# Kernel tuning notes

Hardware: AMD Instinct MI355X
Metric: run time of the kernel (lower is better)

The kernel has to match this reference:

```python
import jax, jax.numpy as jnp
import numpy as np

B, L, V, H = 2, 2048, 1024, 16
HD = V // H  # head size 64
EPS = 1e-3   # keras LayerNormalization default


def setup_inputs() -> dict:
    key = jax.random.key(0)
    ks = jax.random.split(key, 10)
    scale = 1.0 / np.sqrt(V)
    return {
        "query": jax.random.normal(ks[0], (B, L, V), jnp.float32),
        "key_t": jax.random.normal(ks[1], (B, L, V), jnp.float32),
        "value": jax.random.normal(ks[2], (B, L, V), jnp.float32),
        "Wq": jax.random.normal(ks[3], (H, V, HD), jnp.float32) * scale,
        "Wk": jax.random.normal(ks[4], (H, V, HD), jnp.float32) * scale,
        "Wv": jax.random.normal(ks[5], (H, V, HD), jnp.float32) * scale,
        "gamma": jnp.ones((V,), jnp.float32),
        "beta": jnp.zeros((V,), jnp.float32),
        "query_mask": jax.random.randint(ks[6], (B, L), 0, 2, jnp.int32),
        "value_mask": jax.random.randint(ks[7], (B, L), 0, 2, jnp.int32),
    }


def reference(query, key_t, value, Wq, Wk, Wv, gamma, beta, query_mask, value_mask):
    qm = query_mask.astype(jnp.float32)  # (B,L)
    vm = value_mask.astype(jnp.float32)  # (B,L)

    # per-head no-bias Dense projections, batched over heads
    Q = jnp.einsum('blv,hvd->bhld', query, Wq)
    K = jnp.einsum('blv,hvd->bhld', key_t, Wk)
    Vh = jnp.einsum('blv,hvd->bhld', value, Wv)

    scores = jnp.einsum('bhld,bhmd->bhlm', Q, K) / jnp.sqrt(jnp.float32(HD))
    attn = jax.nn.softmax(scores, axis=-1)

    # post-softmax multiplicative masking (faithful to original)
    tri = jnp.tril(jnp.ones((L, L), jnp.float32))  # (L,L) causal
    attn = attn * tri[None, None, :, :]
    attn = attn * qm[:, None, :, None] * vm[:, None, None, :]

    heads = jnp.einsum('bhlm,bhmd->bhld', attn, Vh)
    x = heads.transpose(0, 2, 1, 3).reshape(B, L, V)  # concat heads

    # dropout is identity at inference
    y = x + query
    mu = jnp.mean(y, axis=-1, keepdims=True)
    var = jnp.mean((y - mu) ** 2, axis=-1, keepdims=True)
    return gamma * (y - mu) * jax.lax.rsqrt(var + EPS) + beta
```

## Files before the change

### kernel.cpp

```cpp
#include <hip/hip_runtime.h>
#include <math.h>

constexpr int NB = 2;
constexpr int SL = 2048;
constexpr int NV = 1024;
constexpr int NH = 16;
constexpr int DH = 64;
constexpr float LN_EPS = 1e-3f;

typedef __bf16 bf16_t;
typedef __bf16 v8bf __attribute__((ext_vector_type(8)));
typedef float  v4f  __attribute__((ext_vector_type(4)));

__device__ __forceinline__ v8bf cvt8(float4 a, float4 b) {
  v8bf v;
  v[0] = (bf16_t)a.x; v[1] = (bf16_t)a.y; v[2] = (bf16_t)a.z; v[3] = (bf16_t)a.w;
  v[4] = (bf16_t)b.x; v[5] = (bf16_t)b.y; v[6] = (bf16_t)b.z; v[7] = (bf16_t)b.w;
  return v;
}
__device__ __forceinline__ unsigned pack_bf16(float a, float b) {
  unsigned short ua = __builtin_bit_cast(unsigned short, (bf16_t)a);
  unsigned short ub = __builtin_bit_cast(unsigned short, (bf16_t)b);
  return (unsigned)ua | ((unsigned)ub << 16);
}
__device__ __forceinline__ void async_cp16(const void* g, void* l) {
  __builtin_amdgcn_global_load_lds(
      (const __attribute__((address_space(1))) unsigned int*)g,
      (__attribute__((address_space(3))) unsigned int*)l, 16, 0, 0);
}

__global__ __launch_bounds__(256)
void wcvt(const float* __restrict__ Wq, const float* __restrict__ Wk,
          const float* __restrict__ Wv, bf16_t* __restrict__ Wt) {
  __shared__ float ls[64][65];
  const int z = blockIdx.z;
  const float* W = z == 0 ? Wq : (z == 1 ? Wk : Wv);
  const float sc = z == 0 ? 0.125f * 1.44269504f : 1.0f;
  const int h = blockIdx.y, v0 = blockIdx.x * 64;
  const int t = threadIdx.x;
  const int rr = t >> 4, c4 = t & 15;
  const float* src = W + ((size_t)h * NV + v0) * DH;
#pragma unroll
  for (int it = 0; it < 4; ++it) {
    float4 f = *(const float4*)(src + (size_t)(rr + it * 16) * DH + c4 * 4);
    ls[rr + it * 16][c4 * 4 + 0] = f.x;
    ls[rr + it * 16][c4 * 4 + 1] = f.y;
    ls[rr + it * 16][c4 * 4 + 2] = f.z;
    ls[rr + it * 16][c4 * 4 + 3] = f.w;
  }
  __syncthreads();
  const int dd = t >> 2, vq = t & 3;
  bf16_t tmp[16];
#pragma unroll
  for (int i = 0; i < 16; ++i) tmp[i] = (bf16_t)(ls[vq * 16 + i][dd] * sc);
  bf16_t* dst = Wt + ((size_t)z * NV + h * 64 + dd) * NV + v0 + vq * 16;
  *(v8bf*)dst = *(v8bf*)&tmp[0];
  *(v8bf*)(dst + 8) = *(v8bf*)&tmp[8];
}

__global__ __launch_bounds__(256, 3)
void proj_mfma(const float* __restrict__ A0, const float* __restrict__ A1,
               const float* __restrict__ A2, const bf16_t* __restrict__ Wtb,
               const int* __restrict__ vmask,
               bf16_t* __restrict__ O0, bf16_t* __restrict__ O1,
               bf16_t* __restrict__ O2) {
  __shared__ __align__(16) float  Asb[2][128 * 32];
  __shared__ __align__(16) bf16_t Wsb[2][128 * 32];

  const int z = blockIdx.z;
  const float*  A   = z == 0 ? A0 : (z == 1 ? A1 : A2);
  bf16_t*       out = z == 0 ? O0 : (z == 1 ? O1 : O2);
  const bf16_t* W   = Wtb + (size_t)z * NV * NV;

  const int t = threadIdx.x, w = t >> 6, lane = t & 63;
  const int g = lane >> 4, lx = lane & 15;
  const int m0 = blockIdx.x * 128, n0 = blockIdx.y * 128;
  const int rbase = (w >> 1) * 64, cbase = (w & 1) * 64;

  {
    const int ph = blockIdx.x % 3;
    if (ph == 1)      __builtin_amdgcn_s_sleep(26);
    else if (ph == 2) __builtin_amdgcn_s_sleep(52);
  }
  const int kph = blockIdx.x & 31;

  auto stageA = [&](int k0, int buf) {
#pragma unroll
    for (int s = 0; s < 4; ++s) {
      const int r = w * 32 + s * 8 + (lane >> 3);
      const int c = (lane & 7) ^ (r & 7);
      async_cp16(A + (size_t)(m0 + r) * NV + k0 + c * 4,
                 (char*)Asb[buf] + (w * 32 + s * 8) * 128);
    }
  };
  auto stageW = [&](int k0, int buf) {
#pragma unroll
    for (int s = 0; s < 2; ++s) {
      const int r = w * 32 + s * 16 + (lane >> 2);
      const int c = (lane & 3) ^ (r & 3);
      async_cp16(W + (size_t)(n0 + r) * NV + k0 + c * 8,
                 (char*)Wsb[buf] + (w * 32 + s * 16) * 64);
    }
  };
  auto kof = [&](int it) { return ((it + kph) & 31) * 32; };

  v4f acc[4][4] = {};
  stageA(kof(0), 0);
  stageW(kof(0), 0);

  for (int it = 0; it < 32; ++it) {
    const int buf = it & 1;
    __syncthreads();
    if (it < 31) { stageA(kof(it + 1), buf ^ 1); stageW(kof(it + 1), buf ^ 1); }
    v8bf af[4], wf[4];
#pragma unroll
    for (int rt = 0; rt < 4; ++rt) {
      const int row = rbase + rt * 16 + lx;
      const int sw = row & 7;
      float4 f0 = *(const float4*)((const char*)Asb[buf] + row * 128 + (((2 * g)     ^ sw) * 16));
      float4 f1 = *(const float4*)((const char*)Asb[buf] + row * 128 + (((2 * g + 1) ^ sw) * 16));
      af[rt] = cvt8(f0, f1);
    }
#pragma unroll
    for (int ct = 0; ct < 4; ++ct) {
      const int row = cbase + ct * 16 + lx;
      wf[ct] = *(const v8bf*)((const char*)Wsb[buf] + row * 64 +
                              ((g ^ (row & 3)) * 16));
    }
#pragma unroll
    for (int rt = 0; rt < 4; ++rt)
#pragma unroll
      for (int ct = 0; ct < 4; ++ct)
        acc[rt][ct] = __builtin_amdgcn_mfma_f32_16x16x32_bf16(
            af[rt], wf[ct], acc[rt][ct], 0, 0, 0);
  }

  if (z < 2) {
#pragma unroll
    for (int rt = 0; rt < 4; ++rt) {
#pragma unroll
      for (int reg = 0; reg < 4; ++reg) {
        const int row = m0 + rbase + rt * 16 + g * 4 + reg;
        const int b = row >> 11, l = row & (SL - 1);
#pragma unroll
        for (int ct = 0; ct < 4; ++ct) {
          const int n = n0 + cbase + ct * 16 + lx;
          const int h = n >> 6, d = n & 63;
          out[((size_t)(b * NH + h) * SL + l) * DH + d] = (bf16_t)acc[rt][ct][reg];
        }
      }
    }
  } else {
#pragma unroll
    for (int rt = 0; rt < 4; ++rt) {
      const int row = m0 + rbase + rt * 16 + g * 4;
      const int b = row >> 11, l = row & (SL - 1);
      float vm0 = (float)vmask[b * SL + l + 0];
      float vm1 = (float)vmask[b * SL + l + 1];
      float vm2 = (float)vmask[b * SL + l + 2];
      float vm3 = (float)vmask[b * SL + l + 3];
#pragma unroll
      for (int ct = 0; ct < 4; ++ct) {
        const int n = n0 + cbase + ct * 16 + lx;
        const int h = n >> 6, d = n & 63;
        uint2 u = {pack_bf16(acc[rt][ct][0] * vm0, acc[rt][ct][1] * vm1),
                   pack_bf16(acc[rt][ct][2] * vm2, acc[rt][ct][3] * vm3)};
        *(uint2*)&out[((size_t)(b * NH + h) * DH + d) * SL + l] = u;
      }
    }
  }
}

__global__ __launch_bounds__(256, 3)
void attn_mfma(const bf16_t* __restrict__ Qg, const bf16_t* __restrict__ Kg,
               const bf16_t* __restrict__ Vtg_all, const int* __restrict__ qmask,
               float* __restrict__ Xout) {
  __shared__ __align__(16) bf16_t kbuf[2][64 * 64];
  __shared__ __align__(16) bf16_t vbuf[2][64 * 64];
  __shared__ __align__(16) bf16_t Ps[4][32][72];

  const int id = blockIdx.x;
  const int bh = (id & 7) | ((id >> 7) << 3);
  const int qb = 15 - ((id >> 3) & 15);
  const int t = threadIdx.x, w = t >> 6, lane = t & 63;
  const int g = lane >> 4, lx = lane & 15;
  const int b = bh >> 4, h = bh & 15;
  const int l0 = qb * 128;
  const int lastAct = 2 * qb + 1;

  if ((id >> 3) & 1) __builtin_amdgcn_s_sleep(32);

  const bf16_t* Kb  = Kg + (size_t)bh * SL * DH;
  const bf16_t* Vtg = Vtg_all + (size_t)bh * DH * SL;

  v8bf qf[2][2];
#pragma unroll
  for (int qt = 0; qt < 2; ++qt)
#pragma unroll
    for (int ks = 0; ks < 2; ++ks)
      qf[qt][ks] = *(const v8bf*)&Qg[((size_t)bh * SL + l0 + w * 32 + qt * 16 + lx) * DH +
                                     ks * 32 + g * 8];

  v4f O[2][4] = {};
  float suml[2] = {0.f, 0.f};

  const int sr_off = lane >> 3, sc_l = lane & 7;
  auto stageK = [&](int mb, int buf) {
#pragma unroll
    for (int s = 0; s < 2; ++s) {
      const int r = w * 16 + s * 8 + sr_off;
      const int c = sc_l ^ (r & 7);
      async_cp16(Kb + (size_t)(mb + r) * DH + c * 8,
                 (char*)kbuf[buf] + (w * 16 + s * 8) * 128);
    }
  };
  auto stageV = [&](int mb, int buf) {
#pragma unroll
    for (int s = 0; s < 2; ++s) {
      const int r = w * 16 + s * 8 + sr_off;
      const int c = sc_l ^ (r & 7);
      async_cp16(Vtg + (size_t)r * SL + mb + c * 8,
                 (char*)vbuf[buf] + (w * 16 + s * 8) * 128);
    }
  };

  stageK(0, 0);
  stageV(0, 0);

  for (int mt = 0; mt <= lastAct; ++mt) {
    const int pb = mt & 1;
    __syncthreads();
    if (mt < SL / 64 - 1)  stageK((mt + 1) * 64, pb ^ 1);
    if (mt + 1 <= lastAct) stageV((mt + 1) * 64, pb ^ 1);

    v4f S[4][2];
#pragma unroll
    for (int mt2 = 0; mt2 < 4; ++mt2) {
      S[mt2][0] = (v4f){0.f, 0.f, 0.f, 0.f};
      S[mt2][1] = (v4f){0.f, 0.f, 0.f, 0.f};
    }
#pragma unroll
    for (int ks = 0; ks < 2; ++ks)
#pragma unroll
      for (int mt2 = 0; mt2 < 4; ++mt2) {
        const int row = mt2 * 16 + lx;
        v8bf kf = *(const v8bf*)((const char*)kbuf[pb] + row * 128 +
                                 (((ks * 4 + g) ^ (lx & 7)) * 16));
#pragma unroll
        for (int qt = 0; qt < 2; ++qt)
          S[mt2][qt] = __builtin_amdgcn_mfma_f32_16x16x32_bf16(
              kf, qf[qt][ks], S[mt2][qt], 0, 0, 0);
      }

    const bool diagzone = (mt >= 2 * qb);
#pragma unroll
    for (int mt2 = 0; mt2 < 4; ++mt2)
#pragma unroll
      for (int qt = 0; qt < 2; ++qt) {
        float e0 = __builtin_amdgcn_exp2f(S[mt2][qt][0]);
        float e1 = __builtin_amdgcn_exp2f(S[mt2][qt][1]);
        float e2 = __builtin_amdgcn_exp2f(S[mt2][qt][2]);
        float e3 = __builtin_amdgcn_exp2f(S[mt2][qt][3]);
        suml[qt] += (e0 + e1) + (e2 + e3);
        if (diagzone) {
          const int ml = mt * 64 + mt2 * 16 + g * 4;
          const int ql = l0 + w * 32 + qt * 16 + lx;
          e0 = (ml + 0 <= ql) ? e0 : 0.f;
          e1 = (ml + 1 <= ql) ? e1 : 0.f;
          e2 = (ml + 2 <= ql) ? e2 : 0.f;
          e3 = (ml + 3 <= ql) ? e3 : 0.f;
        }
        uint2 u = {pack_bf16(e0, e1), pack_bf16(e2, e3)};
        *(uint2*)&Ps[w][qt * 16 + lx][mt2 * 16 + g * 4] = u;
      }

#pragma unroll
    for (int ks = 0; ks < 2; ++ks) {
      v8bf pf[2];
#pragma unroll
      for (int qt = 0; qt < 2; ++qt)
        pf[qt] = *(const v8bf*)&Ps[w][qt * 16 + lx][ks * 32 + g * 8];
#pragma unroll
      for (int dt = 0; dt < 4; ++dt) {
        const int row = dt * 16 + lx;
        v8bf vf = *(const v8bf*)((const char*)vbuf[pb] + row * 128 +
                                 (((ks * 4 + g) ^ (lx & 7)) * 16));
#pragma unroll
        for (int qt = 0; qt < 2; ++qt)
          O[qt][dt] = __builtin_amdgcn_mfma_f32_16x16x32_bf16(
              pf[qt], vf, O[qt][dt], 0, 0, 0);
      }
    }
  }

  for (int mt = lastAct + 1; mt < SL / 64; ++mt) {
    const int pb = mt & 1;
    __syncthreads();
    if (mt < SL / 64 - 1) stageK((mt + 1) * 64, pb ^ 1);
    v4f S[4][2];
#pragma unroll
    for (int mt2 = 0; mt2 < 4; ++mt2) {
      S[mt2][0] = (v4f){0.f, 0.f, 0.f, 0.f};
      S[mt2][1] = (v4f){0.f, 0.f, 0.f, 0.f};
    }
#pragma unroll
    for (int ks = 0; ks < 2; ++ks)
#pragma unroll
      for (int mt2 = 0; mt2 < 4; ++mt2) {
        const int row = mt2 * 16 + lx;
        v8bf kf = *(const v8bf*)((const char*)kbuf[pb] + row * 128 +
                                 (((ks * 4 + g) ^ (lx & 7)) * 16));
#pragma unroll
        for (int qt = 0; qt < 2; ++qt)
          S[mt2][qt] = __builtin_amdgcn_mfma_f32_16x16x32_bf16(
              kf, qf[qt][ks], S[mt2][qt], 0, 0, 0);
      }
#pragma unroll
    for (int mt2 = 0; mt2 < 4; ++mt2)
#pragma unroll
      for (int qt = 0; qt < 2; ++qt)
        suml[qt] += (__builtin_amdgcn_exp2f(S[mt2][qt][0]) +
                     __builtin_amdgcn_exp2f(S[mt2][qt][1])) +
                    (__builtin_amdgcn_exp2f(S[mt2][qt][2]) +
                     __builtin_amdgcn_exp2f(S[mt2][qt][3]));
  }

  suml[0] += __shfl_xor(suml[0], 16); suml[0] += __shfl_xor(suml[0], 32);
  suml[1] += __shfl_xor(suml[1], 16); suml[1] += __shfl_xor(suml[1], 32);
#pragma unroll
  for (int qt = 0; qt < 2; ++qt) {
#pragma unroll
    for (int reg = 0; reg < 4; ++reg) {
      const int q = l0 + w * 32 + qt * 16 + g * 4 + reg;
      const float den = __shfl(suml[qt], g * 4 + reg);
      const float inv = (float)qmask[b * SL + q] / den;
#pragma unroll
      for (int dt = 0; dt < 4; ++dt)
        Xout[((size_t)(b * SL + q)) * NV + h * DH + dt * 16 + lx] =
            O[qt][dt][reg] * inv;
    }
  }
}

__global__ __launch_bounds__(256)
void ln_kernel(const float* __restrict__ X, const float* __restrict__ query,
               const float* __restrict__ gamma, const float* __restrict__ beta,
               float* __restrict__ out) {
  const int row0 = blockIdx.x * 2;
  const int t = threadIdx.x;
  float4 gv = *(const float4*)(gamma + t * 4);
  float4 bv = *(const float4*)(beta + t * 4);
  float y[2][4];
  float s[2], ss[2];
#pragma unroll
  for (int r = 0; r < 2; ++r) {
    float4 xv = *(const float4*)(X + (size_t)(row0 + r) * NV + t * 4);
    float4 qv = *(const float4*)(query + (size_t)(row0 + r) * NV + t * 4);
    y[r][0] = xv.x + qv.x; y[r][1] = xv.y + qv.y;
    y[r][2] = xv.z + qv.z; y[r][3] = xv.w + qv.w;
    s[r]  = (y[r][0] + y[r][1]) + (y[r][2] + y[r][3]);
    ss[r] = (y[r][0]*y[r][0] + y[r][1]*y[r][1]) + (y[r][2]*y[r][2] + y[r][3]*y[r][3]);
  }
#pragma unroll
  for (int off = 1; off < 64; off <<= 1) {
    s[0]  += __shfl_xor(s[0], off);  ss[0] += __shfl_xor(ss[0], off);
    s[1]  += __shfl_xor(s[1], off);  ss[1] += __shfl_xor(ss[1], off);
  }
  __shared__ float wsum[2][2][4];
  const int wid = t >> 6;
  if ((t & 63) == 0) {
    wsum[0][0][wid] = s[0]; wsum[0][1][wid] = ss[0];
    wsum[1][0][wid] = s[1]; wsum[1][1][wid] = ss[1];
  }
  __syncthreads();
#pragma unroll
  for (int r = 0; r < 2; ++r) {
    float sr  = (wsum[r][0][0] + wsum[r][0][1]) + (wsum[r][0][2] + wsum[r][0][3]);
    float ssr = (wsum[r][1][0] + wsum[r][1][1]) + (wsum[r][1][2] + wsum[r][1][3]);
    const float mu   = sr * (1.f / NV);
    const float var  = ssr * (1.f / NV) - mu * mu;
    const float rstd = rsqrtf(var + LN_EPS);
    float4 o;
    o.x = gv.x * (y[r][0] - mu) * rstd + bv.x;
    o.y = gv.y * (y[r][1] - mu) * rstd + bv.y;
    o.z = gv.z * (y[r][2] - mu) * rstd + bv.z;
    o.w = gv.w * (y[r][3] - mu) * rstd + bv.w;
    *(float4*)(out + (size_t)(row0 + r) * NV + t * 4) = o;
  }
}

extern "C" void kernel_launch(void* const* d_in, const int* in_sizes, int n_in,
                              void* d_out, int out_size, void* d_ws, size_t ws_size,
                              hipStream_t stream) {
  const float* query = (const float*)d_in[0];
  const float* key_t = (const float*)d_in[1];
  const float* value = (const float*)d_in[2];
  const float* Wq    = (const float*)d_in[3];
  const float* Wk    = (const float*)d_in[4];
  const float* Wv    = (const float*)d_in[5];
  const float* gamma = (const float*)d_in[6];
  const float* beta  = (const float*)d_in[7];
  const int*   qmask = (const int*)d_in[8];
  const int*   vmask = (const int*)d_in[9];
  float* out = (float*)d_out;

  const size_t per = (size_t)NB * NH * SL * DH;
  bf16_t* Qws = (bf16_t*)d_ws;
  bf16_t* Kws = Qws + per;
  bf16_t* Vws = Kws + per;
  bf16_t* Wtb = Vws + per;

  wcvt<<<dim3(16, 16, 3), 256, 0, stream>>>(Wq, Wk, Wv, Wtb);
  proj_mfma<<<dim3(32, 8, 3), 256, 0, stream>>>(query, key_t, value, Wtb,
                                                vmask, Qws, Kws, Vws);
  attn_mfma<<<512, 256, 0, stream>>>(Qws, Kws, Vws, qmask, out);
  ln_kernel<<<NB * SL / 2, 256, 0, stream>>>(out, query, gamma, beta, out);
}
```

Measured before the change: 230.8 us.

## Pre-convert activations to bf16 in a separate kernel before projection GEMM

```diff
diff --git a/kernel.cpp b/kernel.cpp
--- a/kernel.cpp
+++ b/kernel.cpp
@@ -12,12 +12,6 @@
 typedef __bf16 v8bf __attribute__((ext_vector_type(8)));
 typedef float  v4f  __attribute__((ext_vector_type(4)));
 
-__device__ __forceinline__ v8bf cvt8(float4 a, float4 b) {
-  v8bf v;
-  v[0] = (bf16_t)a.x; v[1] = (bf16_t)a.y; v[2] = (bf16_t)a.z; v[3] = (bf16_t)a.w;
-  v[4] = (bf16_t)b.x; v[5] = (bf16_t)b.y; v[6] = (bf16_t)b.z; v[7] = (bf16_t)b.w;
-  return v;
-}
 __device__ __forceinline__ unsigned pack_bf16(float a, float b) {
   unsigned short ua = __builtin_bit_cast(unsigned short, (bf16_t)a);
   unsigned short ub = __builtin_bit_cast(unsigned short, (bf16_t)b);
@@ -27,6 +21,19 @@
   __builtin_amdgcn_global_load_lds(
       (const __attribute__((address_space(1))) unsigned int*)g,
       (__attribute__((address_space(3))) unsigned int*)l, 16, 0, 0);
+}
+
+__global__ __launch_bounds__(256)
+void acvt(const float* __restrict__ q, const float* __restrict__ k,
+          const float* __restrict__ v, bf16_t* __restrict__ oq,
+          bf16_t* __restrict__ ok, bf16_t* __restrict__ ov) {
+  const int z = blockIdx.y;
+  const float* src = z == 0 ? q : (z == 1 ? k : v);
+  bf16_t*      dst = z == 0 ? oq : (z == 1 ? ok : ov);
+  const size_t i = ((size_t)blockIdx.x * 256 + threadIdx.x) * 4;
+  float4 f = *(const float4*)(src + i);
+  uint2 u = {pack_bf16(f.x, f.y), pack_bf16(f.z, f.w)};
+  *(uint2*)(dst + i) = u;
 }
 
 __global__ __launch_bounds__(256)
@@ -58,17 +65,17 @@
   *(v8bf*)(dst + 8) = *(v8bf*)&tmp[8];
 }
 
-__global__ __launch_bounds__(256, 3)
-void proj_mfma(const float* __restrict__ A0, const float* __restrict__ A1,
-               const float* __restrict__ A2, const bf16_t* __restrict__ Wtb,
+__global__ __launch_bounds__(256, 4)
+void proj_mfma(const bf16_t* __restrict__ A0, const bf16_t* __restrict__ A1,
+               const bf16_t* __restrict__ A2, const bf16_t* __restrict__ Wtb,
                const int* __restrict__ vmask,
                bf16_t* __restrict__ O0, bf16_t* __restrict__ O1,
                bf16_t* __restrict__ O2) {
-  __shared__ __align__(16) float  Asb[2][128 * 32];
+  __shared__ __align__(16) bf16_t Asb[2][128 * 32];
   __shared__ __align__(16) bf16_t Wsb[2][128 * 32];
 
   const int z = blockIdx.z;
-  const float*  A   = z == 0 ? A0 : (z == 1 ? A1 : A2);
+  const bf16_t* A   = z == 0 ? A0 : (z == 1 ? A1 : A2);
   bf16_t*       out = z == 0 ? O0 : (z == 1 ? O1 : O2);
   const bf16_t* W   = Wtb + (size_t)z * NV * NV;
 
@@ -77,49 +84,44 @@
   const int m0 = blockIdx.x * 128, n0 = blockIdx.y * 128;
   const int rbase = (w >> 1) * 64, cbase = (w & 1) * 64;
 
-  {
-    const int ph = blockIdx.x % 3;
-    if (ph == 1)      __builtin_amdgcn_s_sleep(26);
-    else if (ph == 2) __builtin_amdgcn_s_sleep(52);
-  }
-  const int kph = blockIdx.x & 31;
-
+  const int sr = lane >> 2;
+  const int sc = (lane & 3);
   auto stageA = [&](int k0, int buf) {
 #pragma unroll
-    for (int s = 0; s < 4; ++s) {
-      const int r = w * 32 + s * 8 + (lane >> 3);
-      const int c = (lane & 7) ^ (r & 7);
-      async_cp16(A + (size_t)(m0 + r) * NV + k0 + c * 4,
-                 (char*)Asb[buf] + (w * 32 + s * 8) * 128);
+    for (int s = 0; s < 2; ++s) {
+      const int r = w * 32 + s * 16 + sr;
+      const int c = sc ^ (r & 3);
+      async_cp16(A + (size_t)(m0 + r) * NV + k0 + c * 8,
+                 (char*)Asb[buf] + (w * 32 + s * 16) * 64);
     }
   };
   auto stageW = [&](int k0, int buf) {
 #pragma unroll
     for (int s = 0; s < 2; ++s) {
-      const int r = w * 32 + s * 16 + (lane >> 2);
-      const int c = (lane & 3) ^ (r & 3);
+      const int r = w * 32 + s * 16 + sr;
+      const int c = sc ^ (r & 3);
       async_cp16(W + (size_t)(n0 + r) * NV + k0 + c * 8,
                  (char*)Wsb[buf] + (w * 32 + s * 16) * 64);
     }
   };
-  auto kof = [&](int it) { return ((it + kph) & 31) * 32; };
 
   v4f acc[4][4] = {};
-  stageA(kof(0), 0);
-  stageW(kof(0), 0);
+  stageA(0, 0);
+  stageW(0, 0);
 
   for (int it = 0; it < 32; ++it) {
     const int buf = it & 1;
     __syncthreads();
-    if (it < 31) { stageA(kof(it + 1), buf ^ 1); stageW(kof(it + 1), buf ^ 1); }
+    if (it < 31) {
+      stageA((it + 1) * 32, buf ^ 1);
+      stageW((it + 1) * 32, buf ^ 1);
+    }
     v8bf af[4], wf[4];
 #pragma unroll
     for (int rt = 0; rt < 4; ++rt) {
       const int row = rbase + rt * 16 + lx;
-      const int sw = row & 7;
-      float4 f0 = *(const float4*)((const char*)Asb[buf] + row * 128 + (((2 * g)     ^ sw) * 16));
-      float4 f1 = *(const float4*)((const char*)Asb[buf] + row * 128 + (((2 * g + 1) ^ sw) * 16));
-      af[rt] = cvt8(f0, f1);
+      af[rt] = *(const v8bf*)((const char*)Asb[buf] + row * 64 +
+                              ((g ^ (row & 3)) * 16));
     }
 #pragma unroll
     for (int ct = 0; ct < 4; ++ct) {
@@ -187,8 +189,6 @@
   const int b = bh >> 4, h = bh & 15;
   const int l0 = qb * 128;
   const int lastAct = 2 * qb + 1;
-
-  if ((id >> 3) & 1) __builtin_amdgcn_s_sleep(32);
 
   const bf16_t* Kb  = Kg + (size_t)bh * SL * DH;
   const bf16_t* Vtg = Vtg_all + (size_t)bh * DH * SL;
@@ -409,9 +409,14 @@
   bf16_t* Kws = Qws + per;
   bf16_t* Vws = Kws + per;
   bf16_t* Wtb = Vws + per;
-
+  bf16_t* Aq  = Wtb + (size_t)3 * NV * NV;
+  bf16_t* Ak  = Aq + per;
+  bf16_t* Av  = Ak + per;
+
+  acvt<<<dim3((NB * SL * NV) / (256 * 4), 3), 256, 0, stream>>>(
+      query, key_t, value, Aq, Ak, Av);
   wcvt<<<dim3(16, 16, 3), 256, 0, stream>>>(Wq, Wk, Wv, Wtb);
-  proj_mfma<<<dim3(32, 8, 3), 256, 0, stream>>>(query, key_t, value, Wtb,
+  proj_mfma<<<dim3(32, 8, 3), 256, 0, stream>>>(Aq, Ak, Av, Wtb,
                                                 vmask, Qws, Kws, Vws);
   attn_mfma<<<512, 256, 0, stream>>>(Qws, Kws, Vws, qmask, out);
   ln_kernel<<<NB * SL / 2, 256, 0, stream>>>(out, query, gamma, beta, out);
```

After: 209.5 us. 9.3% less time.
